# Performance work log

Measured on AMD Instinct MI355X. Metric: run time of the kernel, lower is better.

The kernel has to match this reference:

```python
import jax, jax.numpy as jnp
import numpy as np

B, L, DMQ, DMV = 8, 1024, 512, 512
H, DK, DV, DOUT = 8, 64, 64, 512
EPS = 1e-6


def _layer_norm(x, gamma, beta):
    # LayerNorm over last dim (size H*DK or H*DV), eps=1e-6
    mu = jnp.mean(x, axis=-1, keepdims=True)
    var = jnp.mean(jnp.square(x - mu), axis=-1, keepdims=True)
    return (x - mu) * jax.lax.rsqrt(var + EPS) * gamma + beta


def setup_inputs() -> dict:
    key = jax.random.key(0)
    ks = jax.random.split(key, 20)
    s = 0.02
    return {
        "q": jax.random.normal(ks[0], (B, L, DMQ), jnp.float32),
        "k": jax.random.normal(ks[1], (B, L, DMV), jnp.float32),
        "v": jax.random.normal(ks[2], (B, L, DMV), jnp.float32),
        "Wq": jax.random.normal(ks[3], (DMQ, H * DK), jnp.float32) * s,
        "bq": jnp.zeros((H * DK,), jnp.float32),
        "Wk": jax.random.normal(ks[4], (DMV, H * DK), jnp.float32) * s,
        "bk": jnp.zeros((H * DK,), jnp.float32),
        "Wv": jax.random.normal(ks[5], (DMV, H * DV), jnp.float32) * s,
        "bv": jnp.zeros((H * DV,), jnp.float32),
        "g_q": jnp.ones((H * DK,), jnp.float32),
        "be_q": jnp.zeros((H * DK,), jnp.float32),
        "g_k": jnp.ones((H * DK,), jnp.float32),
        "be_k": jnp.zeros((H * DK,), jnp.float32),
        "g_v": jnp.ones((H * DV,), jnp.float32),
        "be_v": jnp.zeros((H * DV,), jnp.float32),
        "W1": jax.random.normal(ks[6], (H * DV, H * DV), jnp.float32) * s,
        "b1": jnp.zeros((H * DV,), jnp.float32),
        "W2": jax.random.normal(ks[7], (H * DV, DOUT), jnp.float32) * s,
        "b2": jnp.zeros((DOUT,), jnp.float32),
    }


def reference(q, k, v, Wq, bq, Wk, bk, Wv, bv, g_q, be_q, g_k, be_k, g_v, be_v, W1, b1, W2, b2):
    b, lq = q.shape[0], q.shape[1]
    qp = q @ Wq + bq                       # [B, Lq, H*DK]
    kp = k @ Wk + bk                       # [B, Lk, H*DK]
    vp = v @ Wv + bv                       # [B, Lv, H*DV]
    residual = qp.reshape(b, lq, H, DK)
    qn = _layer_norm(qp, g_q, be_q).reshape(b, lq, H, DK)
    kn = _layer_norm(kp, g_k, be_k).reshape(b, -1, H, DK)
    vn = _layer_norm(vp, g_v, be_v).reshape(b, -1, H, DV)
    # scaled dot-product attention (mask=None path)
    scores = jnp.einsum("bqhd,bkhd->bhqk", qn, kn) / jnp.sqrt(jnp.float32(DK))
    attn = jax.nn.softmax(scores, axis=-1)
    out = jnp.einsum("bhqk,bkhd->bqhd", attn, vn).reshape(b, lq, H * DV)
    # 2-layer FFN head: fc1 (ReLU) then fc2
    h = jax.nn.relu(out @ W1 + b1)
    out = h @ W2 + b2                      # [B, Lq, DOUT]
    return (out, residual)
```

## Files before the change

kernel.cpp:

```cpp
#include <hip/hip_runtime.h>
#include <hip/hip_bf16.h>
#include <stdint.h>

typedef unsigned short u16;
typedef __attribute__((ext_vector_type(8))) short bf16x8;
typedef __attribute__((ext_vector_type(4))) float f32x4;
typedef __attribute__((ext_vector_type(16))) float f32x16;

#define NR 8192
#define DM 512
#define NH 8
#define HD 64
#define LQ 1024

#define QSCALE (0.125f * 1.4426950408889634f)
#define SOFF 16.0f

__device__ __forceinline__ u16 f2b(float f) {
    union { float f; uint32_t u; } v; v.f = f;
    uint32_t r = v.u + 0x7fffu + ((v.u >> 16) & 1u);
    return (u16)(r >> 16);
}
__device__ __forceinline__ uint32_t pk2(float lo, float hi) {
    __hip_bfloat162 h = __float22bfloat162_rn(make_float2(lo, hi));
    union { __hip_bfloat162 h; uint32_t u; } c; c.h = h;
    return c.u;
}

__global__ __launch_bounds__(256)
void conv3_kernel(const float* __restrict__ q, const float* __restrict__ k,
                  const float* __restrict__ v, u16* __restrict__ qo,
                  u16* __restrict__ ko, u16* __restrict__ vo)
{
    const int y = blockIdx.y;
    const float* in = y == 0 ? q : y == 1 ? k : v;
    u16* out = y == 0 ? qo : y == 1 ? ko : vo;
    const int i = blockIdx.x * 256 + threadIdx.x;
    const float4* p = (const float4*)in + (size_t)i * 2;
    float4 a = p[0], b = p[1];
    uint4 o;
    o.x = pk2(a.x, a.y);
    o.y = pk2(a.z, a.w);
    o.z = pk2(b.x, b.y);
    o.w = pk2(b.z, b.w);
    ((uint4*)out)[i] = o;
}

__global__ __launch_bounds__(256)
void wt5_kernel(const float* __restrict__ W0, const float* __restrict__ W1,
                const float* __restrict__ W2, const float* __restrict__ W3,
                const float* __restrict__ W4,
                u16* __restrict__ T0, u16* __restrict__ T1, u16* __restrict__ T2,
                u16* __restrict__ T3, u16* __restrict__ T4)
{
    const int z = blockIdx.z;
    const float* W = z == 0 ? W0 : z == 1 ? W1 : z == 2 ? W2 : z == 3 ? W3 : W4;
    u16* Wt = z == 0 ? T0 : z == 1 ? T1 : z == 2 ? T2 : z == 3 ? T3 : T4;

    __shared__ float S[64][65];
    const int k0 = blockIdx.x * 64, n0 = blockIdx.y * 64;
    #pragma unroll
    for (int p = 0; p < 16; ++p) {
        int idx = threadIdx.x + p * 256;
        int r = idx >> 6, c = idx & 63;
        S[r][c] = W[(size_t)(k0 + r) * DM + n0 + c];
    }
    __syncthreads();
    #pragma unroll
    for (int p = 0; p < 16; ++p) {
        int idx = threadIdx.x + p * 256;
        int r = idx >> 6, c = idx & 63;
        Wt[(size_t)(n0 + r) * DM + k0 + c] = f2b(S[c][r]);
    }
}

__global__ __launch_bounds__(256)
void vt_kernel(const u16* __restrict__ vn, u16* __restrict__ vt)
{
    __shared__ u16 S[64][82];
    const int lt = blockIdx.x, bh = blockIdx.y;
    const int b = bh >> 3, h = bh & 7;
    const int t = threadIdx.x;
    {
        const int r = t >> 2, dc = (t & 3) * 16;
        const u16* src = vn + (size_t)(b * LQ + lt * 64 + r) * DM + h * HD + dc;
        *(uint4*)&S[r][dc]     = *(const uint4*)(src);
        *(uint4*)&S[r][dc + 8] = *(const uint4*)(src + 8);
    }
    __syncthreads();
    {
        const int d = t >> 2, lc = (t & 3) * 16;
        u16 tmp[16];
        #pragma unroll
        for (int e = 0; e < 16; ++e) tmp[e] = S[lc + e][d];
        u16* dst = vt + (((size_t)bh * HD + d) << 10) + lt * 64 + lc;
        *(uint4*)dst       = *(uint4*)&tmp[0];
        *(uint4*)(dst + 8) = *(uint4*)&tmp[8];
    }
}

__global__ __launch_bounds__(256)
void ln3_kernel(const float* __restrict__ Pq, const float* __restrict__ Pk,
                const float* __restrict__ Pv,
                const float* __restrict__ gq, const float* __restrict__ bq,
                const float* __restrict__ gk, const float* __restrict__ bk,
                const float* __restrict__ gv, const float* __restrict__ bv,
                u16* __restrict__ oq, u16* __restrict__ ok, u16* __restrict__ ov)
{
    const int y = blockIdx.y;
    const float* P  = y == 0 ? Pq : y == 1 ? Pk : Pv;
    const float* gm = y == 0 ? gq : y == 1 ? gk : gv;
    const float* be = y == 0 ? bq : y == 1 ? bk : bv;
    u16* out = y == 0 ? oq : y == 1 ? ok : ov;
    const float scale = y == 0 ? QSCALE : 1.f;

    const int row = blockIdx.x, t = threadIdx.x;
    const size_t off = (size_t)row * DM + t * 2;
    float2 v = *(const float2*)(P + off);
    float s = v.x + v.y, s2 = v.x * v.x + v.y * v.y;
    #pragma unroll
    for (int o = 32; o; o >>= 1) { s += __shfl_down(s, o); s2 += __shfl_down(s2, o); }
    __shared__ float ss[4], ss2[4];
    if ((t & 63) == 0) { ss[t >> 6] = s; ss2[t >> 6] = s2; }
    __syncthreads();
    float S = ss[0] + ss[1] + ss[2] + ss[3];
    float S2 = ss2[0] + ss2[1] + ss2[2] + ss2[3];
    float mu = S * (1.f / DM);
    float var = S2 * (1.f / DM) - mu * mu;
    float rs = rsqrtf(var + 1e-6f);
    float g0 = gm[t * 2] * scale, g1 = gm[t * 2 + 1] * scale;
    float b0 = be[t * 2] * scale, b1 = be[t * 2 + 1] * scale;
    float o0 = (v.x - mu) * rs * g0 + b0;
    float o1 = (v.y - mu) * rs * g1 + b1;
    *(uint32_t*)(out + off) = pk2(o0, o1);
}

template<bool RELU, bool OUT_BF16>
__device__ __forceinline__
void gemm_body(const u16* __restrict__ A, const u16* __restrict__ Bt,
               const float* __restrict__ bias, void* __restrict__ Cout)
{
    __shared__ u16 Al[4 * 128 * 8];
    __shared__ u16 Bl[4 * 128 * 8];
    const int t = threadIdx.x;
    const int w = t >> 6, l = t & 63;
    const int m0 = blockIdx.x * 128, n0 = blockIdx.y * 128;
    const int sg = w & 3, sr = (w >> 2) * 64;
    const int wm = w >> 2, wn = w & 3;

    const u16* Ap = A  + (size_t)(m0 + sr + l) * DM + sg * 8;
    const u16* Bp = Bt + (size_t)(n0 + sr + l) * DM + sg * 8;
    const int su = (sg * 128 + sr + l) * 8;

    uint4 ga = *(const uint4*)Ap;
    uint4 gb = *(const uint4*)Bp;

    f32x4 acc[4][2];
    #pragma unroll
    for (int mi = 0; mi < 4; ++mi)
        #pragma unroll
        for (int ni = 0; ni < 2; ++ni)
            acc[mi][ni] = {0.f, 0.f, 0.f, 0.f};

    for (int kb = 0; kb < DM / 32; ++kb) {
        __syncthreads();
        *(uint4*)&Al[su] = ga;
        *(uint4*)&Bl[su] = gb;
        if (kb + 1 < DM / 32) {
            ga = *(const uint4*)(Ap + (kb + 1) * 32);
            gb = *(const uint4*)(Bp + (kb + 1) * 32);
        }
        __syncthreads();
        bf16x8 af[4], bfr[2];
        #pragma unroll
        for (int mi = 0; mi < 4; ++mi)
            af[mi] = *(const bf16x8*)&Al[((l >> 4) * 128 + wm * 64 + mi * 16 + (l & 15)) * 8];
        #pragma unroll
        for (int ni = 0; ni < 2; ++ni)
            bfr[ni] = *(const bf16x8*)&Bl[((l >> 4) * 128 + wn * 32 + ni * 16 + (l & 15)) * 8];
        #pragma unroll
        for (int mi = 0; mi < 4; ++mi)
            #pragma unroll
            for (int ni = 0; ni < 2; ++ni)
                acc[mi][ni] = __builtin_amdgcn_mfma_f32_16x16x32_bf16(af[mi], bfr[ni], acc[mi][ni], 0, 0, 0);
    }

    const int cq = l >> 4, cr = l & 15;
    #pragma unroll
    for (int mi = 0; mi < 4; ++mi) {
        const int row = m0 + wm * 64 + mi * 16 + cq * 4;
        #pragma unroll
        for (int ni = 0; ni < 2; ++ni) {
            const int col = n0 + wn * 32 + ni * 16 + cr;
            const float bb = bias[col];
            #pragma unroll
            for (int j = 0; j < 4; ++j) {
                float vv = acc[mi][ni][j] + bb;
                if (RELU) vv = fmaxf(vv, 0.f);
                if (OUT_BF16) ((u16*)Cout)[(size_t)(row + j) * DM + col] = f2b(vv);
                else          ((float*)Cout)[(size_t)(row + j) * DM + col] = vv;
            }
        }
    }
}

template<bool RELU, bool OUT_BF16>
__global__ __launch_bounds__(512)
void mfma_gemm_kernel(const u16* __restrict__ A, const u16* __restrict__ Bt,
                      const float* __restrict__ bias, void* __restrict__ Cout)
{
    gemm_body<RELU, OUT_BF16>(A, Bt, bias, Cout);
}

__global__ __launch_bounds__(512)
void gemm_qkv_kernel(const u16* __restrict__ qbf, const u16* __restrict__ kbf,
                     const u16* __restrict__ vbf,
                     const u16* __restrict__ WqT, const u16* __restrict__ WkT,
                     const u16* __restrict__ WvT,
                     const float* __restrict__ bq, const float* __restrict__ bk,
                     const float* __restrict__ bv,
                     float* __restrict__ res, float* __restrict__ kp,
                     float* __restrict__ vp)
{
    const int z = blockIdx.z;
    const u16* A    = z == 0 ? qbf : z == 1 ? kbf : vbf;
    const u16* Bt   = z == 0 ? WqT : z == 1 ? WkT : WvT;
    const float* bb = z == 0 ? bq  : z == 1 ? bk  : bv;
    void* C         = z == 0 ? (void*)res : z == 1 ? (void*)kp : (void*)vp;
    gemm_body<false, false>(A, Bt, bb, C);
}

__global__ __launch_bounds__(512, 2)
void attn_mfma_kernel(const u16* __restrict__ qn, const u16* __restrict__ kn,
                      const u16* __restrict__ vt, u16* __restrict__ ab)
{
    __shared__ u16 Kl[2][8 * 64 * 8];
    __shared__ u16 Pl[8][8 * 32 * 8];

    const int t = threadIdx.x;
    const int w = t >> 6, l = t & 63;
    const int hi = l >> 5, ln = l & 31;
    const int qt = blockIdx.x, h = blockIdx.y, b = blockIdx.z;
    const size_t bbase = (size_t)b * LQ * DM + h * HD;
    const int q0 = qt * 256 + w * 32;

    bf16x8 qf[4];
    {
        const u16* qp = qn + bbase + (size_t)(q0 + ln) * DM + hi * 8;
        #pragma unroll
        for (int c = 0; c < 4; ++c)
            qf[c] = *(const bf16x8*)(qp + c * 16);
    }

    const u16* Vb = vt + ((((size_t)(b * NH + h)) * HD + ln) << 10);
    const u16* Kg = kn + bbase + (size_t)l * DM + w * 8;
    u16* Pw = &Pl[w][0];

    f32x16 oa0, oa1;
    #pragma unroll
    for (int r = 0; r < 16; ++r) { oa0[r] = 0.f; oa1[r] = 0.f; }
    float lsum = 0.f;

    *(uint4*)&Kl[0][t * 8] = *(const uint4*)Kg;
    uint4 ka = *(const uint4*)(Kg + (size_t)64 * DM);
    int cur = 0;

    for (int kt = 0; kt < 16; ++kt) {
        __syncthreads();

        uint4 vfr[4][2];
        #pragma unroll
        for (int ks = 0; ks < 4; ++ks)
            #pragma unroll
            for (int dh = 0; dh < 2; ++dh)
                vfr[ks][dh] = *(const uint4*)(Vb + (((size_t)dh * 32) << 10)
                                              + kt * 64 + ks * 16 + hi * 8);

        f32x16 sa0, sa1;
        #pragma unroll
        for (int r = 0; r < 16; ++r) { sa0[r] = -SOFF; sa1[r] = -SOFF; }
        #pragma unroll
        for (int c = 0; c < 4; ++c) {
            bf16x8 k0 = *(const bf16x8*)&Kl[cur][((c * 2 + hi) * 64 + ln) * 8];
            bf16x8 k1 = *(const bf16x8*)&Kl[cur][((c * 2 + hi) * 64 + 32 + ln) * 8];
            sa0 = __builtin_amdgcn_mfma_f32_32x32x16_bf16(k0, qf[c], sa0, 0, 0, 0);
            sa1 = __builtin_amdgcn_mfma_f32_32x32x16_bf16(k1, qf[c], sa1, 0, 0, 0);
        }

        if (kt < 15) {
            *(uint4*)&Kl[cur ^ 1][t * 8] = ka;
            if (kt < 14) ka = *(const uint4*)(Kg + (size_t)(kt + 2) * 64 * DM);
        }

        #pragma unroll
        for (int r = 0; r < 16; ++r) {
            sa0[r] = __builtin_amdgcn_exp2f(sa0[r]);
            sa1[r] = __builtin_amdgcn_exp2f(sa1[r]);
            lsum += sa0[r] + sa1[r];
        }

        #pragma unroll
        for (int g0 = 0; g0 < 4; ++g0) {
            uint2 w0, w1;
            w0.x = pk2(sa0[4 * g0],     sa0[4 * g0 + 1]);
            w0.y = pk2(sa0[4 * g0 + 2], sa0[4 * g0 + 3]);
            w1.x = pk2(sa1[4 * g0],     sa1[4 * g0 + 1]);
            w1.y = pk2(sa1[4 * g0 + 2], sa1[4 * g0 + 3]);
            *(uint2*)&Pw[(g0 * 32 + ln) * 8 + 4 * hi]       = w0;
            *(uint2*)&Pw[((g0 + 4) * 32 + ln) * 8 + 4 * hi] = w1;
        }

        #pragma unroll
        for (int ks = 0; ks < 4; ++ks) {
            bf16x8 pa = *(const bf16x8*)&Pw[((ks * 2 + hi) * 32 + ln) * 8];
            union { uint4 u; bf16x8 v; } v0, v1;
            v0.u = vfr[ks][0]; v1.u = vfr[ks][1];
            oa0 = __builtin_amdgcn_mfma_f32_32x32x16_bf16(v0.v, pa, oa0, 0, 0, 0);
            oa1 = __builtin_amdgcn_mfma_f32_32x32x16_bf16(v1.v, pa, oa1, 0, 0, 0);
        }
        cur ^= 1;
    }

    lsum += __shfl_xor(lsum, 32, 64);
    const float rinv = 1.f / lsum;
    u16* op = ab + (size_t)(b * LQ + q0 + ln) * DM + h * HD;
    #pragma unroll
    for (int g = 0; g < 4; ++g) {
        uint2 s0, s1;
        s0.x = pk2(oa0[4 * g] * rinv, oa0[4 * g + 1] * rinv);
        s0.y = pk2(oa0[4 * g + 2] * rinv, oa0[4 * g + 3] * rinv);
        s1.x = pk2(oa1[4 * g] * rinv, oa1[4 * g + 1] * rinv);
        s1.y = pk2(oa1[4 * g + 2] * rinv, oa1[4 * g + 3] * rinv);
        *(uint2*)(op + 8 * g + 4 * hi)      = s0;
        *(uint2*)(op + 32 + 8 * g + 4 * hi) = s1;
    }
}

extern "C" void kernel_launch(void* const* d_in, const int* in_sizes, int n_in,
                              void* d_out, int out_size, void* d_ws, size_t ws_size,
                              hipStream_t stream)
{
    const float* q    = (const float*)d_in[0];
    const float* k    = (const float*)d_in[1];
    const float* v    = (const float*)d_in[2];
    const float* Wq   = (const float*)d_in[3];
    const float* bq   = (const float*)d_in[4];
    const float* Wk   = (const float*)d_in[5];
    const float* bk   = (const float*)d_in[6];
    const float* Wv   = (const float*)d_in[7];
    const float* bv   = (const float*)d_in[8];
    const float* g_q  = (const float*)d_in[9];
    const float* be_q = (const float*)d_in[10];
    const float* g_k  = (const float*)d_in[11];
    const float* be_k = (const float*)d_in[12];
    const float* g_v  = (const float*)d_in[13];
    const float* be_v = (const float*)d_in[14];
    const float* W1   = (const float*)d_in[15];
    const float* b1   = (const float*)d_in[16];
    const float* W2   = (const float*)d_in[17];
    const float* b2   = (const float*)d_in[18];

    float* outp = (float*)d_out;
    float* res  = outp + (size_t)NR * DM;

    char* wsb = (char*)d_ws;
    const size_t MB = 1024 * 1024;
    float* kp  = (float*)(wsb);
    float* vp  = (float*)(wsb + 16 * MB);
    u16* qbf = (u16*)(wsb + 32 * MB);
    u16* kbf = (u16*)(wsb + 40 * MB);
    u16* vbf = (u16*)(wsb + 48 * MB);
    u16* WqT = (u16*)(wsb + 56 * MB);
    u16* WkT = WqT + 512 * 512;
    u16* WvT = WkT + 512 * 512;
    u16* W1T = WvT + 512 * 512;
    u16* W2T = W1T + 512 * 512;
    u16* abb = (u16*)kp;
    u16* hbb = (u16*)vp;
    u16* vtb = (u16*)(wsb + 24 * MB);

    conv3_kernel<<<dim3(2048, 3), 256, 0, stream>>>(q, k, v, qbf, kbf, vbf);

    wt5_kernel<<<dim3(8, 8, 5), 256, 0, stream>>>(Wq, Wk, Wv, W1, W2,
                                                  WqT, WkT, WvT, W1T, W2T);

    gemm_qkv_kernel<<<dim3(NR / 128, DM / 128, 3), 512, 0, stream>>>(
        qbf, kbf, vbf, WqT, WkT, WvT, bq, bk, bv, res, kp, vp);

    ln3_kernel<<<dim3(NR, 3), 256, 0, stream>>>(res, kp, vp,
                                                g_q, be_q, g_k, be_k, g_v, be_v,
                                                qbf, kbf, vbf);

    vt_kernel<<<dim3(16, 64), 256, 0, stream>>>(vbf, vtb);

    attn_mfma_kernel<<<dim3(LQ / 256, NH, 8), 512, 0, stream>>>(qbf, kbf, vtb, abb);

    dim3 gg(NR / 128, DM / 128);
    mfma_gemm_kernel<true,  true ><<<gg, 512, 0, stream>>>(abb, W1T, b1, (void*)hbb);
    mfma_gemm_kernel<false, false><<<gg, 512, 0, stream>>>(hbb, W2T, b2, (void*)outp);
}
```

Baseline: 144.6 us.

## Halve block size for GEMM and attention kernels to raise block count

GEMM blocks shrink from 512 to 256 threads with 128x64 output tiles, doubling grid size. Attention blocks drop to 4 waves covering 128 queries and launch as a flat 512-block grid with a remapped block index that groups batch/head pairs. The goal is more blocks per CU and better load balance across the many CUs, at the cost of more redundant K/V and weight loads per output.

After: 164.5 us. 13.8% more time.

```diff
diff --git a/kernel.cpp b/kernel.cpp
--- a/kernel.cpp
+++ b/kernel.cpp
@@ -141,19 +141,18 @@
                const float* __restrict__ bias, void* __restrict__ Cout)
 {
     __shared__ u16 Al[4 * 128 * 8];
-    __shared__ u16 Bl[4 * 128 * 8];
+    __shared__ u16 Bl[4 * 64 * 8];
     const int t = threadIdx.x;
     const int w = t >> 6, l = t & 63;
-    const int m0 = blockIdx.x * 128, n0 = blockIdx.y * 128;
-    const int sg = w & 3, sr = (w >> 2) * 64;
-    const int wm = w >> 2, wn = w & 3;
-
-    const u16* Ap = A  + (size_t)(m0 + sr + l) * DM + sg * 8;
-    const u16* Bp = Bt + (size_t)(n0 + sr + l) * DM + sg * 8;
-    const int su = (sg * 128 + sr + l) * 8;
-
-    uint4 ga = *(const uint4*)Ap;
-    uint4 gb = *(const uint4*)Bp;
+    const int m0 = blockIdx.x * 128, n0 = blockIdx.y * 64;
+    const int wm = w >> 1, wn = w & 1;
+
+    const u16* Ap = A + (size_t)(m0 + (t & 127)) * DM + (t >> 7) * 8;
+    const u16* Bp = Bt + (size_t)(n0 + (t & 63)) * DM + (t >> 6) * 8;
+
+    uint4 ga1 = *(const uint4*)Ap;
+    uint4 ga2 = *(const uint4*)(Ap + 16);
+    uint4 gb  = *(const uint4*)Bp;
 
     f32x4 acc[4][2];
     #pragma unroll
@@ -164,11 +163,13 @@
 
     for (int kb = 0; kb < DM / 32; ++kb) {
         __syncthreads();
-        *(uint4*)&Al[su] = ga;
-        *(uint4*)&Bl[su] = gb;
+        *(uint4*)&Al[t * 8]          = ga1;
+        *(uint4*)&Al[(t + 256) * 8]  = ga2;
+        *(uint4*)&Bl[t * 8]          = gb;
         if (kb + 1 < DM / 32) {
-            ga = *(const uint4*)(Ap + (kb + 1) * 32);
-            gb = *(const uint4*)(Bp + (kb + 1) * 32);
+            ga1 = *(const uint4*)(Ap + (kb + 1) * 32);
+            ga2 = *(const uint4*)(Ap + (kb + 1) * 32 + 16);
+            gb  = *(const uint4*)(Bp + (kb + 1) * 32);
         }
         __syncthreads();
         bf16x8 af[4], bfr[2];
@@ -177,7 +178,7 @@
             af[mi] = *(const bf16x8*)&Al[((l >> 4) * 128 + wm * 64 + mi * 16 + (l & 15)) * 8];
         #pragma unroll
         for (int ni = 0; ni < 2; ++ni)
-            bfr[ni] = *(const bf16x8*)&Bl[((l >> 4) * 128 + wn * 32 + ni * 16 + (l & 15)) * 8];
+            bfr[ni] = *(const bf16x8*)&Bl[((l >> 4) * 64 + wn * 32 + ni * 16 + (l & 15)) * 8];
         #pragma unroll
         for (int mi = 0; mi < 4; ++mi)
             #pragma unroll
@@ -205,14 +206,14 @@
 }
 
 template<bool RELU, bool OUT_BF16>
-__global__ __launch_bounds__(512)
+__global__ __launch_bounds__(256, 4)
 void mfma_gemm_kernel(const u16* __restrict__ A, const u16* __restrict__ Bt,
                       const float* __restrict__ bias, void* __restrict__ Cout)
 {
     gemm_body<RELU, OUT_BF16>(A, Bt, bias, Cout);
 }
 
-__global__ __launch_bounds__(512)
+__global__ __launch_bounds__(256, 4)
 void gemm_qkv_kernel(const u16* __restrict__ qbf, const u16* __restrict__ kbf,
                      const u16* __restrict__ vbf,
                      const u16* __restrict__ WqT, const u16* __restrict__ WkT,
@@ -230,19 +231,25 @@
     gemm_body<false, false>(A, Bt, bb, C);
 }
 
-__global__ __launch_bounds__(512, 2)
+__global__ __launch_bounds__(256, 4)
 void attn_mfma_kernel(const u16* __restrict__ qn, const u16* __restrict__ kn,
                       const u16* __restrict__ vt, u16* __restrict__ ab)
 {
     __shared__ u16 Kl[2][8 * 64 * 8];
-    __shared__ u16 Pl[8][8 * 32 * 8];
+    __shared__ u16 Pl[4][8 * 32 * 8];
 
     const int t = threadIdx.x;
     const int w = t >> 6, l = t & 63;
     const int hi = l >> 5, ln = l & 31;
-    const int qt = blockIdx.x, h = blockIdx.y, b = blockIdx.z;
+
+    const int bid = blockIdx.x;
+    const int slot = bid >> 3;
+    const int bh = (bid & 7) + 8 * (slot & 7);
+    const int qt = slot >> 3;
+    const int b = bh >> 3, h = bh & 7;
+
     const size_t bbase = (size_t)b * LQ * DM + h * HD;
-    const int q0 = qt * 256 + w * 32;
+    const int q0 = qt * 128 + w * 32;
 
     bf16x8 qf[4];
     {
@@ -252,8 +259,8 @@
             qf[c] = *(const bf16x8*)(qp + c * 16);
     }
 
-    const u16* Vb = vt + ((((size_t)(b * NH + h)) * HD + ln) << 10);
-    const u16* Kg = kn + bbase + (size_t)l * DM + w * 8;
+    const u16* Vb = vt + (((size_t)bh * HD + ln) << 10);
+    const u16* Kg = kn + bbase + (size_t)(t & 63) * DM + (t >> 6) * 8;
     u16* Pw = &Pl[w][0];
 
     f32x16 oa0, oa1;
@@ -261,8 +268,10 @@
     for (int r = 0; r < 16; ++r) { oa0[r] = 0.f; oa1[r] = 0.f; }
     float lsum = 0.f;
 
-    *(uint4*)&Kl[0][t * 8] = *(const uint4*)Kg;
-    uint4 ka = *(const uint4*)(Kg + (size_t)64 * DM);
+    *(uint4*)&Kl[0][t * 8]         = *(const uint4*)Kg;
+    *(uint4*)&Kl[0][(t + 256) * 8] = *(const uint4*)(Kg + 32);
+    uint4 ka1 = *(const uint4*)(Kg + (size_t)64 * DM);
+    uint4 ka2 = *(const uint4*)(Kg + (size_t)64 * DM + 32);
     int cur = 0;
 
     for (int kt = 0; kt < 16; ++kt) {
@@ -288,8 +297,12 @@
         }
 
         if (kt < 15) {
-            *(uint4*)&Kl[cur ^ 1][t * 8] = ka;
-            if (kt < 14) ka = *(const uint4*)(Kg + (size_t)(kt + 2) * 64 * DM);
+            *(uint4*)&Kl[cur ^ 1][t * 8]         = ka1;
+            *(uint4*)&Kl[cur ^ 1][(t + 256) * 8] = ka2;
+            if (kt < 14) {
+                ka1 = *(const uint4*)(Kg + (size_t)(kt + 2) * 64 * DM);
+                ka2 = *(const uint4*)(Kg + (size_t)(kt + 2) * 64 * DM + 32);
+            }
         }
 
         #pragma unroll
@@ -384,7 +397,7 @@
     wt5_kernel<<<dim3(8, 8, 5), 256, 0, stream>>>(Wq, Wk, Wv, W1, W2,
                                                   WqT, WkT, WvT, W1T, W2T);
 
-    gemm_qkv_kernel<<<dim3(NR / 128, DM / 128, 3), 512, 0, stream>>>(
+    gemm_qkv_kernel<<<dim3(NR / 128, DM / 64, 3), 256, 0, stream>>>(
         qbf, kbf, vbf, WqT, WkT, WvT, bq, bk, bv, res, kp, vp);
 
     ln3_kernel<<<dim3(NR, 3), 256, 0, stream>>>(res, kp, vp,
@@ -393,9 +406,9 @@
 
     vt_kernel<<<dim3(16, 64), 256, 0, stream>>>(vbf, vtb);
 
-    attn_mfma_kernel<<<dim3(LQ / 256, NH, 8), 512, 0, stream>>>(qbf, kbf, vtb, abb);
-
-    dim3 gg(NR / 128, DM / 128);
-    mfma_gemm_kernel<true,  true ><<<gg, 512, 0, stream>>>(abb, W1T, b1, (void*)hbb);
-    mfma_gemm_kernel<false, false><<<gg, 512, 0, stream>>>(hbb, W2T, b2, (void*)outp);
-}
+    attn_mfma_kernel<<<512, 256, 0, stream>>>(qbf, kbf, vtb, abb);
+
+    dim3 gg(NR / 128, DM / 64);
+    mfma_gemm_kernel<true,  true ><<<gg, 256, 0, stream>>>(abb, W1T, b1, (void*)hbb);
+    mfma_gemm_kernel<false, false><<<gg, 256, 0, stream>>>(hbb, W2T, b2, (void*)outp);
+}
```

## Stage V tiles in LDS and shrink attention blocks to 128 queries

Applied to the files above, without the earlier changes.

Each attention block now has 4 waves covering 128 queries instead of 8 waves covering 256. V tiles are staged cooperatively through double-buffered shared memory, like K, rather than each wave loading V fragments straight from global memory. The 1D grid is remapped so that consecutive blocks cover different batch/head pairs, and launch bounds change to 256 threads with 3 blocks per CU. This cuts redundant per-wave global V traffic and raises the number of blocks, at the cost of more LDS traffic and K/V reloads across twice as many query tiles.

New measurement: 127.7 us. -11.7%, faster.

```diff
diff --git a/kernel.cpp b/kernel.cpp
--- a/kernel.cpp
+++ b/kernel.cpp
@@ -230,19 +230,26 @@
     gemm_body<false, false>(A, Bt, bb, C);
 }
 
-__global__ __launch_bounds__(512, 2)
+__global__ __launch_bounds__(256, 3)
 void attn_mfma_kernel(const u16* __restrict__ qn, const u16* __restrict__ kn,
                       const u16* __restrict__ vt, u16* __restrict__ ab)
 {
     __shared__ u16 Kl[2][8 * 64 * 8];
-    __shared__ u16 Pl[8][8 * 32 * 8];
+    __shared__ u16 Vl[2][8 * 64 * 8];
+    __shared__ u16 Pl[4][8 * 32 * 8];
 
     const int t = threadIdx.x;
     const int w = t >> 6, l = t & 63;
     const int hi = l >> 5, ln = l & 31;
-    const int qt = blockIdx.x, h = blockIdx.y, b = blockIdx.z;
+
+    const int bid = blockIdx.x;
+    const int slot = bid >> 3;
+    const int bh = (bid & 7) + 8 * (slot & 7);
+    const int qt = slot >> 3;
+    const int b = bh >> 3, h = bh & 7;
+
     const size_t bbase = (size_t)b * LQ * DM + h * HD;
-    const int q0 = qt * 256 + w * 32;
+    const int q0 = qt * 128 + w * 32;
 
     bf16x8 qf[4];
     {
@@ -252,8 +259,10 @@
             qf[c] = *(const bf16x8*)(qp + c * 16);
     }
 
-    const u16* Vb = vt + ((((size_t)(b * NH + h)) * HD + ln) << 10);
-    const u16* Kg = kn + bbase + (size_t)l * DM + w * 8;
+    const u16* Kg = kn + bbase + (size_t)(t & 63) * DM + (t >> 6) * 8;
+    const u16* Vg = vt + (((size_t)bh * HD + (t >> 3)) << 10) + (t & 7) * 8;
+    const int svu1 = ((t & 7) * 64 + (t >> 3)) * 8;
+    const int svu2 = ((t & 7) * 64 + 32 + (t >> 3)) * 8;
     u16* Pw = &Pl[w][0];
 
     f32x16 oa0, oa1;
@@ -261,20 +270,18 @@
     for (int r = 0; r < 16; ++r) { oa0[r] = 0.f; oa1[r] = 0.f; }
     float lsum = 0.f;
 
-    *(uint4*)&Kl[0][t * 8] = *(const uint4*)Kg;
-    uint4 ka = *(const uint4*)(Kg + (size_t)64 * DM);
+    *(uint4*)&Kl[0][t * 8]         = *(const uint4*)Kg;
+    *(uint4*)&Kl[0][(t + 256) * 8] = *(const uint4*)(Kg + 32);
+    *(uint4*)&Vl[0][svu1]          = *(const uint4*)Vg;
+    *(uint4*)&Vl[0][svu2]          = *(const uint4*)(Vg + (32 << 10));
+    uint4 ka1 = *(const uint4*)(Kg + (size_t)64 * DM);
+    uint4 ka2 = *(const uint4*)(Kg + (size_t)64 * DM + 32);
+    uint4 va1 = *(const uint4*)(Vg + 64);
+    uint4 va2 = *(const uint4*)(Vg + (32 << 10) + 64);
     int cur = 0;
 
     for (int kt = 0; kt < 16; ++kt) {
         __syncthreads();
-
-        uint4 vfr[4][2];
-        #pragma unroll
-        for (int ks = 0; ks < 4; ++ks)
-            #pragma unroll
-            for (int dh = 0; dh < 2; ++dh)
-                vfr[ks][dh] = *(const uint4*)(Vb + (((size_t)dh * 32) << 10)
-                                              + kt * 64 + ks * 16 + hi * 8);
 
         f32x16 sa0, sa1;
         #pragma unroll
@@ -288,8 +295,16 @@
         }
 
         if (kt < 15) {
-            *(uint4*)&Kl[cur ^ 1][t * 8] = ka;
-            if (kt < 14) ka = *(const uint4*)(Kg + (size_t)(kt + 2) * 64 * DM);
+            *(uint4*)&Kl[cur ^ 1][t * 8]         = ka1;
+            *(uint4*)&Kl[cur ^ 1][(t + 256) * 8] = ka2;
+            *(uint4*)&Vl[cur ^ 1][svu1]          = va1;
+            *(uint4*)&Vl[cur ^ 1][svu2]          = va2;
+            if (kt < 14) {
+                ka1 = *(const uint4*)(Kg + (size_t)(kt + 2) * 64 * DM);
+                ka2 = *(const uint4*)(Kg + (size_t)(kt + 2) * 64 * DM + 32);
+                va1 = *(const uint4*)(Vg + (kt + 2) * 64);
+                va2 = *(const uint4*)(Vg + (32 << 10) + (kt + 2) * 64);
+            }
         }
 
         #pragma unroll
@@ -313,10 +328,10 @@
         #pragma unroll
         for (int ks = 0; ks < 4; ++ks) {
             bf16x8 pa = *(const bf16x8*)&Pw[((ks * 2 + hi) * 32 + ln) * 8];
-            union { uint4 u; bf16x8 v; } v0, v1;
-            v0.u = vfr[ks][0]; v1.u = vfr[ks][1];
-            oa0 = __builtin_amdgcn_mfma_f32_32x32x16_bf16(v0.v, pa, oa0, 0, 0, 0);
-            oa1 = __builtin_amdgcn_mfma_f32_32x32x16_bf16(v1.v, pa, oa1, 0, 0, 0);
+            bf16x8 v0 = *(const bf16x8*)&Vl[cur][((ks * 2 + hi) * 64 + ln) * 8];
+            bf16x8 v1 = *(const bf16x8*)&Vl[cur][((ks * 2 + hi) * 64 + 32 + ln) * 8];
+            oa0 = __builtin_amdgcn_mfma_f32_32x32x16_bf16(v0, pa, oa0, 0, 0, 0);
+            oa1 = __builtin_amdgcn_mfma_f32_32x32x16_bf16(v1, pa, oa1, 0, 0, 0);
         }
         cur ^= 1;
     }
@@ -393,7 +408,7 @@
 
     vt_kernel<<<dim3(16, 64), 256, 0, stream>>>(vbf, vtb);
 
-    attn_mfma_kernel<<<dim3(LQ / 256, NH, 8), 512, 0, stream>>>(qbf, kbf, vtb, abb);
+    attn_mfma_kernel<<<512, 256, 0, stream>>>(qbf, kbf, vtb, abb);
 
     dim3 gg(NR / 128, DM / 128);
     mfma_gemm_kernel<true,  true ><<<gg, 512, 0, stream>>>(abb, W1T, b1, (void*)hbb);
```
